# Kernel tuning notes

Measured on AMD Instinct MI355X. Metric: run time of the kernel, lower is better.

Reference implementation:

```python
import jax, jax.numpy as jnp
import numpy as np

N = 50000
E = 800000
D_IN = 256
D_OUT = 256
EPS = 1.0 + 1e-06


def setup_inputs() -> dict:
    key = jax.random.key(0)
    ks = jax.random.split(key, 10)
    x = jax.random.normal(ks[0], (N, D_IN), dtype=jnp.float32)
    lower_indices = jax.random.randint(ks[1], (2, E), 0, N, dtype=jnp.int64)
    lower_values = jax.random.uniform(ks[2], (E,), dtype=jnp.float32)
    upper_indices = jax.random.randint(ks[3], (2, E), 0, N, dtype=jnp.int64)
    upper_values = jax.random.uniform(ks[4], (E,), dtype=jnp.float32)
    s = 1.0 / np.sqrt(D_IN)
    W_lower = jax.random.uniform(ks[5], (D_IN, D_OUT), jnp.float32, -s, s)
    att_lower = jax.random.uniform(ks[6], (2 * D_OUT,), jnp.float32, -s, s)
    W_upper = jax.random.uniform(ks[7], (D_IN, D_OUT), jnp.float32, -s, s)
    att_upper = jax.random.uniform(ks[8], (2 * D_OUT,), jnp.float32, -s, s)
    W_lin = jax.random.uniform(ks[9], (D_IN, D_OUT), jnp.float32, -s, s)
    return {"x": x, "lower_indices": lower_indices, "lower_values": lower_values,
            "upper_indices": upper_indices, "upper_values": upper_values,
            "W_lower": W_lower, "att_lower": att_lower,
            "W_upper": W_upper, "att_upper": att_upper, "W_lin": W_lin}


def can_conv(x, indices, values, W, att_weight):
    # x: [N, d_in]; indices: [2, E] (row=target i, col=source j); values: [E]
    n = x.shape[0]
    xm = x @ W                                    # [N, d_out]
    tgt, src = indices[0], indices[1]
    d = xm.shape[1]
    # attention: elu( [x_i ; x_j] . att_weight ) computed without concat
    score = jax.nn.elu(xm @ att_weight[:d])[tgt] + jax.nn.elu(0.0) * 0.0  # placeholder
    score = jax.nn.elu((xm @ att_weight[:d])[tgt] + (xm @ att_weight[d:])[src])  # [E]
    v = score * values                            # attention * neighborhood values
    # sparse row-wise softmax (per target index)
    m = jax.ops.segment_max(v, tgt, num_segments=n)
    e = jnp.exp(v - m[tgt])
    s = jax.ops.segment_sum(e, tgt, num_segments=n)
    a = e / s[tgt]                                # [E]
    # spmm: out[i] = sum_j a_ij * xm[j]
    return jax.ops.segment_sum(a[:, None] * xm[src], tgt, num_segments=n)


def reference(x, lower_indices, lower_values, upper_indices, upper_values,
              W_lower, att_lower, W_upper, att_upper, W_lin):
    lower_x = can_conv(x, lower_indices, lower_values, W_lower, att_lower)
    upper_x = can_conv(x, upper_indices, upper_values, W_upper, att_upper)
    w_x = (x @ W_lin) * EPS
    return jax.nn.relu(lower_x + upper_x + w_x)
```

## Files before the change

kernel.cpp:

```cpp
#include <hip/hip_runtime.h>
#include <hip/hip_bf16.h>


constexpr int N_NODES = 50000;
constexpr int N_EDGES = 800000;
constexpr int D = 256;
constexpr float EPSV = 1.0f + 1e-06f;

typedef __attribute__((ext_vector_type(8))) short short8;
typedef __attribute__((ext_vector_type(4))) float f32x4;

__device__ __forceinline__ unsigned short f2bf(float f) {
    unsigned int b = __float_as_uint(f);
    unsigned int r = (b + 0x7FFFu + ((b >> 16) & 1u)) >> 16;
    return (unsigned short)r;
}
__device__ __forceinline__ float bf2f(unsigned short u) {
    return __uint_as_float(((unsigned int)u) << 16);
}

__global__ __launch_bounds__(256) void cvt_x_kernel(
    const float4* __restrict__ x, ushort4* __restrict__ xb, int n4)
{
    int i = blockIdx.x * 256 + threadIdx.x;
    if (i >= n4) return;
    float4 v = x[i];
    ushort4 o;
    o.x = f2bf(v.x); o.y = f2bf(v.y); o.z = f2bf(v.z); o.w = f2bf(v.w);
    xb[i] = o;
}

__global__ __launch_bounds__(256) void cvt_w_kernel(
    const float* __restrict__ W0, const float* __restrict__ W1,
    const float* __restrict__ W2, unsigned short* __restrict__ wbT)
{
    int z = blockIdx.y;
    const float* W = (z == 0) ? W0 : (z == 1) ? W1 : W2;
    int n = blockIdx.x;
    int k = threadIdx.x;
    wbT[(size_t)z * 65536 + (size_t)n * 256 + k] = f2bf(W[(size_t)k * 256 + n]);
}

__global__ __launch_bounds__(256) void gemm_fused_kernel(
    const unsigned short* __restrict__ xb, const unsigned short* __restrict__ wbT,
    const float* __restrict__ att_l, const float* __restrict__ att_u,
    unsigned short* __restrict__ xml, unsigned short* __restrict__ xmu,
    float* __restrict__ out,
    float* __restrict__ al, float* __restrict__ bl,
    float* __restrict__ au, float* __restrict__ bu, int M)
{
    const int tid = threadIdx.x;
    const int w = tid >> 6, lane = tid & 63;
    const int r16 = lane & 15, g = lane >> 4;
    const int m0 = blockIdx.x * 32;
    const int n0 = w * 64;

    const int ar0 = min(m0 + r16, M - 1);
    const int ar1 = min(m0 + 16 + r16, M - 1);
    const unsigned short* pa0 = xb + (size_t)ar0 * 256 + 8 * g;
    const unsigned short* pa1 = xb + (size_t)ar1 * 256 + 8 * g;
    const unsigned short* pb  = wbT + (size_t)(n0 + r16) * 256 + 8 * g;

    f32x4 acc[3][2][4];
    #pragma unroll
    for (int z = 0; z < 3; ++z)
        #pragma unroll
        for (int mf = 0; mf < 2; ++mf)
            #pragma unroll
            for (int nf = 0; nf < 4; ++nf)
                acc[z][mf][nf] = (f32x4){0.f, 0.f, 0.f, 0.f};

    #pragma unroll
    for (int kt = 0; kt < 256; kt += 32) {
        short8 a0 = *reinterpret_cast<const short8*>(pa0 + kt);
        short8 a1 = *reinterpret_cast<const short8*>(pa1 + kt);
        #pragma unroll
        for (int z = 0; z < 3; ++z) {
            #pragma unroll
            for (int nf = 0; nf < 4; ++nf) {
                short8 bf = *reinterpret_cast<const short8*>(
                    pb + (size_t)z * 65536 + (size_t)nf * 16 * 256 + kt);
                acc[z][0][nf] = __builtin_amdgcn_mfma_f32_16x16x32_bf16(a0, bf, acc[z][0][nf], 0, 0, 0);
                acc[z][1][nf] = __builtin_amdgcn_mfma_f32_16x16x32_bf16(a1, bf, acc[z][1][nf], 0, 0, 0);
            }
        }
    }

    #pragma unroll
    for (int mf = 0; mf < 2; ++mf)
        #pragma unroll
        for (int r = 0; r < 4; ++r) {
            int row = m0 + mf * 16 + g * 4 + r;
            if (row < M) {
                #pragma unroll
                for (int nf = 0; nf < 4; ++nf) {
                    int col = n0 + nf * 16 + r16;
                    xml[(size_t)row * 256 + col] = f2bf(acc[0][mf][nf][r]);
                    xmu[(size_t)row * 256 + col] = f2bf(acc[1][mf][nf][r]);
                    out[(size_t)row * 256 + col] = acc[2][mf][nf][r] * EPSV;
                }
            }
        }

    float attv[2][2][4];
    #pragma unroll
    for (int h = 0; h < 2; ++h)
        #pragma unroll
        for (int nf = 0; nf < 4; ++nf) {
            int c = h * 256 + n0 + nf * 16 + r16;
            attv[0][h][nf] = att_l[c];
            attv[1][h][nf] = att_u[c];
        }

    __shared__ float red[4][32][4];
    #pragma unroll
    for (int mf = 0; mf < 2; ++mf)
        #pragma unroll
        for (int r = 0; r < 4; ++r) {
            float p[4];
            #pragma unroll
            for (int z = 0; z < 2; ++z)
                #pragma unroll
                for (int h = 0; h < 2; ++h) {
                    float s = 0.f;
                    #pragma unroll
                    for (int nf = 0; nf < 4; ++nf)
                        s += acc[z][mf][nf][r] * attv[z][h][nf];
                    p[z * 2 + h] = s;
                }
            #pragma unroll
            for (int off = 1; off < 16; off <<= 1)
                #pragma unroll
                for (int c = 0; c < 4; ++c)
                    p[c] += __shfl_xor(p[c], off);
            if (r16 == 0) {
                int row_loc = mf * 16 + g * 4 + r;
                red[w][row_loc][0] = p[0];
                red[w][row_loc][1] = p[1];
                red[w][row_loc][2] = p[2];
                red[w][row_loc][3] = p[3];
            }
        }
    __syncthreads();
    if (tid < 128) {
        int row_loc = tid >> 2, comp = tid & 3;
        int row = m0 + row_loc;
        if (row < M) {
            float s = red[0][row_loc][comp] + red[1][row_loc][comp]
                    + red[2][row_loc][comp] + red[3][row_loc][comp];
            float* dst = (comp == 0) ? al : (comp == 1) ? bl : (comp == 2) ? au : bu;
            dst[row] = s;
        }
    }
}

__global__ __launch_bounds__(256) void hist_kernel(
    const int* __restrict__ il, const int* __restrict__ iu,
    int* __restrict__ cl, int* __restrict__ cu,
    int* __restrict__ rkl, int* __restrict__ rku)
{
    int e = blockIdx.x * 256 + threadIdx.x;
    if (e >= N_EDGES) return;
    rkl[e] = atomicAdd(&cl[il[e]], 1);
    rku[e] = atomicAdd(&cu[iu[e]], 1);
}

__global__ __launch_bounds__(1024) void scan_local_kernel(
    const int* __restrict__ cnt0, int* __restrict__ ro0,
    const int* __restrict__ cnt1, int* __restrict__ ro1,
    int* __restrict__ bsum, int n)
{
    int c = blockIdx.y;
    const int* cnt = c ? cnt1 : cnt0;
    int* ro = c ? ro1 : ro0;
    __shared__ int sm[1024];
    int tid = threadIdx.x;
    int i = blockIdx.x * 1024 + tid;
    int v = (i < n) ? cnt[i] : 0;
    sm[tid] = v;
    __syncthreads();
    #pragma unroll
    for (int off = 1; off < 1024; off <<= 1) {
        int t = (tid >= off) ? sm[tid - off] : 0;
        __syncthreads();
        sm[tid] += t;
        __syncthreads();
    }
    if (i < n) ro[i] = sm[tid] - v;
    if (tid == 1023) bsum[c * 64 + blockIdx.x] = sm[1023];
}

__global__ __launch_bounds__(128) void scan_bsum_kernel(int* __restrict__ bsum, int nb)
{
    int c = threadIdx.x >> 6, lane = threadIdx.x & 63;
    int v = (lane < nb) ? bsum[c * 64 + lane] : 0;
    int orig = v;
    #pragma unroll
    for (int off = 1; off < 64; off <<= 1) {
        int t = __shfl_up(v, off);
        if (lane >= off) v += t;
    }
    if (lane < nb) bsum[c * 64 + lane] = v - orig;
}

__global__ __launch_bounds__(256) void scan_apply_kernel(
    int* __restrict__ ro0, int* __restrict__ ro1,
    const int* __restrict__ bsum, int n)
{
    int c = blockIdx.y;
    int* ro = c ? ro1 : ro0;
    int i = blockIdx.x * 256 + threadIdx.x;
    if (i < n) ro[i] += bsum[c * 64 + (i >> 10)];
    if (i == 0) ro[n] = N_EDGES;
}

__global__ __launch_bounds__(256) void scatter_kernel(
    const int* __restrict__ il, const float* __restrict__ vl,
    const int* __restrict__ rol, const int* __restrict__ rkl, int2* __restrict__ egl,
    const int* __restrict__ iu, const float* __restrict__ vu,
    const int* __restrict__ rou, const int* __restrict__ rku, int2* __restrict__ egu)
{
    int e = blockIdx.x * 256 + threadIdx.x;
    if (e >= N_EDGES) return;
    int2 p; p.x = il[N_EDGES + e]; p.y = __float_as_int(vl[e]);
    egl[rol[il[e]] + rkl[e]] = p;
    int2 q; q.x = iu[N_EDGES + e]; q.y = __float_as_int(vu[e]);
    egu[rou[iu[e]] + rku[e]] = q;
}

__device__ __forceinline__ float wave_sum(float v) {
    #pragma unroll
    for (int off = 32; off; off >>= 1) v += __shfl_xor(v, off);
    return v;
}

__device__ __forceinline__ void pv_accum(
    int lane, float invs, float evl, int srcl, int t0, int m,
    const unsigned short* __restrict__ xm, float4& acc)
{
    int t = t0;
    for (; t + 2 <= m; t += 2) {
        float w0 = __shfl(evl, t) * invs;
        int   s0 = __shfl(srcl, t);
        float w1 = __shfl(evl, t + 1) * invs;
        int   s1 = __shfl(srcl, t + 1);
        ushort4 u0 = *reinterpret_cast<const ushort4*>(xm + (size_t)s0 * 256 + lane * 4);
        ushort4 u1 = *reinterpret_cast<const ushort4*>(xm + (size_t)s1 * 256 + lane * 4);
        acc.x += w0 * bf2f(u0.x) + w1 * bf2f(u1.x);
        acc.y += w0 * bf2f(u0.y) + w1 * bf2f(u1.y);
        acc.z += w0 * bf2f(u0.z) + w1 * bf2f(u1.z);
        acc.w += w0 * bf2f(u0.w) + w1 * bf2f(u1.w);
    }
    if (t < m) {
        float w0 = __shfl(evl, t) * invs;
        int   s0 = __shfl(srcl, t);
        ushort4 u0 = *reinterpret_cast<const ushort4*>(xm + (size_t)s0 * 256 + lane * 4);
        acc.x += w0 * bf2f(u0.x);
        acc.y += w0 * bf2f(u0.y);
        acc.z += w0 * bf2f(u0.z);
        acc.w += w0 * bf2f(u0.w);
    }
}

__device__ __forceinline__ void conv_accum(
    int node, int lane,
    const int* __restrict__ ro, const int2* __restrict__ eg,
    const float* __restrict__ a, const float* __restrict__ b,
    const unsigned short* __restrict__ xm, float4& acc)
{
    int rs = ro[node], re = ro[node + 1];
    int deg = re - rs;
    if (deg <= 0) return;
    float ai = a[node];
    if (deg <= 64) {
        float evl = 0.f; int srcl = 0;
        if (lane < deg) {
            int2 p = eg[rs + lane];
            srcl = p.x;
            float xv = ai + b[srcl];
            float sc = (xv > 0.f) ? xv : (expf(xv) - 1.f);
            evl = expf(sc * __int_as_float(p.y));
        }
        float invs = 1.f / wave_sum(evl);
        pv_accum(lane, invs, evl, srcl, 0, deg, xm, acc);
    } else {
        float s = 0.f;
        for (int c = rs; c < re; c += 64) {
            int m = min(64, re - c);
            float evl = 0.f;
            if (lane < m) {
                int2 p = eg[c + lane];
                float xv = ai + b[p.x];
                float sc = (xv > 0.f) ? xv : (expf(xv) - 1.f);
                evl = expf(sc * __int_as_float(p.y));
            }
            s += wave_sum(evl);
        }
        float invs = 1.f / s;
        for (int c = rs; c < re; c += 64) {
            int m = min(64, re - c);
            float evl = 0.f; int srcl = 0;
            if (lane < m) {
                int2 p = eg[c + lane];
                srcl = p.x;
                float xv = ai + b[srcl];
                float sc = (xv > 0.f) ? xv : (expf(xv) - 1.f);
                evl = expf(sc * __int_as_float(p.y));
            }
            pv_accum(lane, invs, evl, srcl, 0, m, xm, acc);
        }
    }
}

__global__ __launch_bounds__(256) void gather_kernel(
    const int* __restrict__ rol, const int2* __restrict__ egl,
    const float* __restrict__ al, const float* __restrict__ bl,
    const unsigned short* __restrict__ xml,
    const int* __restrict__ rou, const int2* __restrict__ egu,
    const float* __restrict__ au, const float* __restrict__ bu,
    const unsigned short* __restrict__ xmu,
    float4* __restrict__ out)
{
    int node = (int)((blockIdx.x * 256 + threadIdx.x) >> 6);
    int lane = threadIdx.x & 63;
    if (node >= N_NODES) return;
    float4 acc = make_float4(0.f, 0.f, 0.f, 0.f);
    conv_accum(node, lane, rol, egl, al, bl, xml, acc);
    conv_accum(node, lane, rou, egu, au, bu, xmu, acc);
    float4 xw = out[(size_t)node * 64 + lane];
    acc.x = fmaxf(acc.x + xw.x, 0.f);
    acc.y = fmaxf(acc.y + xw.y, 0.f);
    acc.z = fmaxf(acc.z + xw.z, 0.f);
    acc.w = fmaxf(acc.w + xw.w, 0.f);
    out[(size_t)node * 64 + lane] = acc;
}

extern "C" void kernel_launch(void* const* d_in, const int* in_sizes, int n_in,
                              void* d_out, int out_size, void* d_ws, size_t ws_size,
                              hipStream_t stream)
{
    (void)in_sizes; (void)n_in; (void)out_size; (void)ws_size;
    const float* x        = (const float*)d_in[0];
    const int*   low_idx  = (const int*)  d_in[1];
    const float* low_vals = (const float*)d_in[2];
    const int*   up_idx   = (const int*)  d_in[3];
    const float* up_vals  = (const float*)d_in[4];
    const float* W_lower  = (const float*)d_in[5];
    const float* att_low  = (const float*)d_in[6];
    const float* W_upper  = (const float*)d_in[7];
    const float* att_up   = (const float*)d_in[8];
    const float* W_lin    = (const float*)d_in[9];
    float* out = (float*)d_out;

    char* ws = (char*)d_ws;
    size_t off = 0;
    auto alloc = [&](size_t bytes) {
        void* p = ws + off;
        off += (bytes + 255) & ~(size_t)255;
        return p;
    };
    unsigned short* xb     = (unsigned short*)alloc((size_t)N_NODES * D * 2);
    unsigned short* wbT    = (unsigned short*)alloc((size_t)3 * 256 * 256 * 2);
    unsigned short* xm_low = (unsigned short*)alloc((size_t)N_NODES * D * 2);
    unsigned short* xm_up  = (unsigned short*)alloc((size_t)N_NODES * D * 2);
    float* a_low  = (float*)alloc(N_NODES * 4);
    float* b_low  = (float*)alloc(N_NODES * 4);
    float* a_up   = (float*)alloc(N_NODES * 4);
    float* b_up   = (float*)alloc(N_NODES * 4);
    int* zero_blk = (int*)alloc(2 * N_NODES * 4);
    int* cnt_low = zero_blk;
    int* cnt_up  = zero_blk + N_NODES;
    int* rk_low  = (int*)alloc((size_t)N_EDGES * 4);
    int* rk_up   = (int*)alloc((size_t)N_EDGES * 4);
    int* ro_low  = (int*)alloc((N_NODES + 1) * 4);
    int* ro_up   = (int*)alloc((N_NODES + 1) * 4);
    int* bsum    = (int*)alloc(2 * 64 * 4);
    int2* eg_low = (int2*)alloc((size_t)N_EDGES * 8);
    int2* eg_up  = (int2*)alloc((size_t)N_EDGES * 8);

    hipMemsetAsync(zero_blk, 0, 2 * N_NODES * 4, stream);

    int n4 = N_NODES * D / 4;
    cvt_x_kernel<<<(n4 + 255) / 256, 256, 0, stream>>>(
        (const float4*)x, (ushort4*)xb, n4);
    dim3 wgrid(256, 3);
    cvt_w_kernel<<<wgrid, 256, 0, stream>>>(W_lower, W_upper, W_lin, wbT);

    int gemmblocks = (N_NODES + 31) / 32;
    gemm_fused_kernel<<<gemmblocks, 256, 0, stream>>>(
        xb, wbT, att_low, att_up, xm_low, xm_up, out,
        a_low, b_low, a_up, b_up, N_NODES);

    int eblocks = (N_EDGES + 255) / 256;
    hist_kernel<<<eblocks, 256, 0, stream>>>(low_idx, up_idx, cnt_low, cnt_up,
                                             rk_low, rk_up);
    dim3 sgrid((N_NODES + 1023) / 1024, 2);
    scan_local_kernel<<<sgrid, 1024, 0, stream>>>(cnt_low, ro_low, cnt_up, ro_up,
                                                  bsum, N_NODES);
    scan_bsum_kernel<<<1, 128, 0, stream>>>(bsum, (N_NODES + 1023) / 1024);
    dim3 agrid((N_NODES + 255) / 256, 2);
    scan_apply_kernel<<<agrid, 256, 0, stream>>>(ro_low, ro_up, bsum, N_NODES);
    scatter_kernel<<<eblocks, 256, 0, stream>>>(
        low_idx, low_vals, ro_low, rk_low, eg_low,
        up_idx,  up_vals,  ro_up,  rk_up,  eg_up);

    int gblocks = (N_NODES + 3) / 4;
    gather_kernel<<<gblocks, 256, 0, stream>>>(
        ro_low, eg_low, a_low, b_low, xm_low,
        ro_up,  eg_up,  a_up,  b_up,  xm_up,
        (float4*)out);
}
```

Measured before the change: 483.5 us.

## Split GEMM per weight with LDS-staged B, separate attention kernel, fuse prep kernels

```diff
diff --git a/kernel.cpp b/kernel.cpp
--- a/kernel.cpp
+++ b/kernel.cpp
@@ -19,150 +19,135 @@
     return __uint_as_float(((unsigned int)u) << 16);
 }
 
-__global__ __launch_bounds__(256) void cvt_x_kernel(
-    const float4* __restrict__ x, ushort4* __restrict__ xb, int n4)
-{
-    int i = blockIdx.x * 256 + threadIdx.x;
-    if (i >= n4) return;
-    float4 v = x[i];
-    ushort4 o;
-    o.x = f2bf(v.x); o.y = f2bf(v.y); o.z = f2bf(v.z); o.w = f2bf(v.w);
-    xb[i] = o;
-}
-
-__global__ __launch_bounds__(256) void cvt_w_kernel(
+__global__ __launch_bounds__(256) void prep_kernel(
+    const float4* __restrict__ x, ushort4* __restrict__ xb, int n4,
     const float* __restrict__ W0, const float* __restrict__ W1,
-    const float* __restrict__ W2, unsigned short* __restrict__ wbT)
-{
-    int z = blockIdx.y;
-    const float* W = (z == 0) ? W0 : (z == 1) ? W1 : W2;
-    int n = blockIdx.x;
-    int k = threadIdx.x;
-    wbT[(size_t)z * 65536 + (size_t)n * 256 + k] = f2bf(W[(size_t)k * 256 + n]);
-}
-
-__global__ __launch_bounds__(256) void gemm_fused_kernel(
+    const float* __restrict__ W2, unsigned short* __restrict__ wbT,
+    const int* __restrict__ il, const int* __restrict__ iu,
+    int* __restrict__ cl, int* __restrict__ cu,
+    int* __restrict__ rkl, int* __restrict__ rku)
+{
+    int gid = blockIdx.x * 256 + threadIdx.x;
+    int gsz = gridDim.x * 256;
+    for (int i = gid; i < n4; i += gsz) {
+        float4 v = x[i];
+        ushort4 o;
+        o.x = f2bf(v.x); o.y = f2bf(v.y); o.z = f2bf(v.z); o.w = f2bf(v.w);
+        xb[i] = o;
+    }
+    for (int i = gid; i < 3 * 65536; i += gsz) {
+        int z = i >> 16, rem = i & 65535;
+        int k = rem >> 8, n = rem & 255;
+        const float* W = (z == 0) ? W0 : (z == 1) ? W1 : W2;
+        wbT[(size_t)z * 65536 + (size_t)n * 256 + k] = f2bf(W[(size_t)k * 256 + n]);
+    }
+    for (int e = gid; e < N_EDGES; e += gsz) {
+        rkl[e] = atomicAdd(&cl[il[e]], 1);
+        rku[e] = atomicAdd(&cu[iu[e]], 1);
+    }
+}
+
+__global__ __launch_bounds__(256) void gemm_lds_kernel(
     const unsigned short* __restrict__ xb, const unsigned short* __restrict__ wbT,
-    const float* __restrict__ att_l, const float* __restrict__ att_u,
     unsigned short* __restrict__ xml, unsigned short* __restrict__ xmu,
-    float* __restrict__ out,
-    float* __restrict__ al, float* __restrict__ bl,
-    float* __restrict__ au, float* __restrict__ bu, int M)
-{
+    float* __restrict__ out, int M)
+{
+    const int wz = blockIdx.z;
     const int tid = threadIdx.x;
     const int w = tid >> 6, lane = tid & 63;
     const int r16 = lane & 15, g = lane >> 4;
-    const int m0 = blockIdx.x * 32;
-    const int n0 = w * 64;
+    const int m0 = blockIdx.x * 128 + w * 32;
+    const int n0 = blockIdx.y * 64;
+
+    __shared__ short8 bs[8][4][64];
+    {
+        const unsigned short* wb = wbT + (size_t)wz * 65536;
+        #pragma unroll
+        for (int c = tid; c < 2048; c += 256) {
+            int kt = c >> 8, nf = (c >> 6) & 3, l = c & 63;
+            bs[kt][nf][l] = *reinterpret_cast<const short8*>(
+                wb + (size_t)(n0 + nf * 16 + (l & 15)) * 256 + kt * 32 + 8 * (l >> 4));
+        }
+    }
+    __syncthreads();
 
     const int ar0 = min(m0 + r16, M - 1);
     const int ar1 = min(m0 + 16 + r16, M - 1);
     const unsigned short* pa0 = xb + (size_t)ar0 * 256 + 8 * g;
     const unsigned short* pa1 = xb + (size_t)ar1 * 256 + 8 * g;
-    const unsigned short* pb  = wbT + (size_t)(n0 + r16) * 256 + 8 * g;
-
-    f32x4 acc[3][2][4];
-    #pragma unroll
-    for (int z = 0; z < 3; ++z)
+
+    f32x4 acc[2][4];
+    #pragma unroll
+    for (int mf = 0; mf < 2; ++mf)
+        #pragma unroll
+        for (int nf = 0; nf < 4; ++nf)
+            acc[mf][nf] = (f32x4){0.f, 0.f, 0.f, 0.f};
+
+    #pragma unroll
+    for (int kt = 0; kt < 8; ++kt) {
+        short8 a0 = *reinterpret_cast<const short8*>(pa0 + kt * 32);
+        short8 a1 = *reinterpret_cast<const short8*>(pa1 + kt * 32);
+        #pragma unroll
+        for (int nf = 0; nf < 4; ++nf) {
+            short8 bf = bs[kt][nf][lane];
+            acc[0][nf] = __builtin_amdgcn_mfma_f32_16x16x32_bf16(a0, bf, acc[0][nf], 0, 0, 0);
+            acc[1][nf] = __builtin_amdgcn_mfma_f32_16x16x32_bf16(a1, bf, acc[1][nf], 0, 0, 0);
+        }
+    }
+
+    if (wz < 2) {
+        unsigned short* dst = wz ? xmu : xml;
         #pragma unroll
         for (int mf = 0; mf < 2; ++mf)
             #pragma unroll
-            for (int nf = 0; nf < 4; ++nf)
-                acc[z][mf][nf] = (f32x4){0.f, 0.f, 0.f, 0.f};
-
-    #pragma unroll
-    for (int kt = 0; kt < 256; kt += 32) {
-        short8 a0 = *reinterpret_cast<const short8*>(pa0 + kt);
-        short8 a1 = *reinterpret_cast<const short8*>(pa1 + kt);
-        #pragma unroll
-        for (int z = 0; z < 3; ++z) {
-            #pragma unroll
-            for (int nf = 0; nf < 4; ++nf) {
-                short8 bf = *reinterpret_cast<const short8*>(
-                    pb + (size_t)z * 65536 + (size_t)nf * 16 * 256 + kt);
-                acc[z][0][nf] = __builtin_amdgcn_mfma_f32_16x16x32_bf16(a0, bf, acc[z][0][nf], 0, 0, 0);
-                acc[z][1][nf] = __builtin_amdgcn_mfma_f32_16x16x32_bf16(a1, bf, acc[z][1][nf], 0, 0, 0);
-            }
-        }
-    }
-
-    #pragma unroll
-    for (int mf = 0; mf < 2; ++mf)
-        #pragma unroll
-        for (int r = 0; r < 4; ++r) {
-            int row = m0 + mf * 16 + g * 4 + r;
-            if (row < M) {
-                #pragma unroll
-                for (int nf = 0; nf < 4; ++nf) {
-                    int col = n0 + nf * 16 + r16;
-                    xml[(size_t)row * 256 + col] = f2bf(acc[0][mf][nf][r]);
-                    xmu[(size_t)row * 256 + col] = f2bf(acc[1][mf][nf][r]);
-                    out[(size_t)row * 256 + col] = acc[2][mf][nf][r] * EPSV;
+            for (int r = 0; r < 4; ++r) {
+                int row = m0 + mf * 16 + g * 4 + r;
+                if (row < M) {
+                    #pragma unroll
+                    for (int nf = 0; nf < 4; ++nf)
+                        dst[(size_t)row * 256 + n0 + nf * 16 + r16] = f2bf(acc[mf][nf][r]);
                 }
             }
-        }
-
-    float attv[2][2][4];
-    #pragma unroll
-    for (int h = 0; h < 2; ++h)
-        #pragma unroll
-        for (int nf = 0; nf < 4; ++nf) {
-            int c = h * 256 + n0 + nf * 16 + r16;
-            attv[0][h][nf] = att_l[c];
-            attv[1][h][nf] = att_u[c];
-        }
-
-    __shared__ float red[4][32][4];
-    #pragma unroll
-    for (int mf = 0; mf < 2; ++mf)
-        #pragma unroll
-        for (int r = 0; r < 4; ++r) {
-            float p[4];
+    } else {
+        #pragma unroll
+        for (int mf = 0; mf < 2; ++mf)
             #pragma unroll
-            for (int z = 0; z < 2; ++z)
-                #pragma unroll
-                for (int h = 0; h < 2; ++h) {
-                    float s = 0.f;
+            for (int r = 0; r < 4; ++r) {
+                int row = m0 + mf * 16 + g * 4 + r;
+                if (row < M) {
                     #pragma unroll
                     for (int nf = 0; nf < 4; ++nf)
-                        s += acc[z][mf][nf][r] * attv[z][h][nf];
-                    p[z * 2 + h] = s;
+                        out[(size_t)row * 256 + n0 + nf * 16 + r16] = acc[mf][nf][r] * EPSV;
                 }
-            #pragma unroll
-            for (int off = 1; off < 16; off <<= 1)
-                #pragma unroll
-                for (int c = 0; c < 4; ++c)
-                    p[c] += __shfl_xor(p[c], off);
-            if (r16 == 0) {
-                int row_loc = mf * 16 + g * 4 + r;
-                red[w][row_loc][0] = p[0];
-                red[w][row_loc][1] = p[1];
-                red[w][row_loc][2] = p[2];
-                red[w][row_loc][3] = p[3];
             }
-        }
-    __syncthreads();
-    if (tid < 128) {
-        int row_loc = tid >> 2, comp = tid & 3;
-        int row = m0 + row_loc;
-        if (row < M) {
-            float s = red[0][row_loc][comp] + red[1][row_loc][comp]
-                    + red[2][row_loc][comp] + red[3][row_loc][comp];
-            float* dst = (comp == 0) ? al : (comp == 1) ? bl : (comp == 2) ? au : bu;
-            dst[row] = s;
-        }
-    }
-}
-
-__global__ __launch_bounds__(256) void hist_kernel(
-    const int* __restrict__ il, const int* __restrict__ iu,
-    int* __restrict__ cl, int* __restrict__ cu,
-    int* __restrict__ rkl, int* __restrict__ rku)
-{
-    int e = blockIdx.x * 256 + threadIdx.x;
-    if (e >= N_EDGES) return;
-    rkl[e] = atomicAdd(&cl[il[e]], 1);
-    rku[e] = atomicAdd(&cu[iu[e]], 1);
+    }
+}
+
+__global__ __launch_bounds__(256) void att_both_kernel(
+    const unsigned short* __restrict__ xml, const unsigned short* __restrict__ xmu,
+    const float* __restrict__ att_l, const float* __restrict__ att_u,
+    float* __restrict__ al, float* __restrict__ bl,
+    float* __restrict__ au, float* __restrict__ bu, int n)
+{
+    int node = (int)((blockIdx.x * 256 + threadIdx.x) >> 6);
+    int lane = threadIdx.x & 63;
+    if (node >= n) return;
+    int o = lane * 4;
+    ushort4 ul = *reinterpret_cast<const ushort4*>(xml + (size_t)node * 256 + o);
+    ushort4 uu = *reinterpret_cast<const ushort4*>(xmu + (size_t)node * 256 + o);
+    float l0 = bf2f(ul.x), l1 = bf2f(ul.y), l2 = bf2f(ul.z), l3 = bf2f(ul.w);
+    float u0 = bf2f(uu.x), u1 = bf2f(uu.y), u2 = bf2f(uu.z), u3 = bf2f(uu.w);
+    float p[4];
+    p[0] = l0 * att_l[o] + l1 * att_l[o + 1] + l2 * att_l[o + 2] + l3 * att_l[o + 3];
+    p[1] = l0 * att_l[D + o] + l1 * att_l[D + o + 1] + l2 * att_l[D + o + 2] + l3 * att_l[D + o + 3];
+    p[2] = u0 * att_u[o] + u1 * att_u[o + 1] + u2 * att_u[o + 2] + u3 * att_u[o + 3];
+    p[3] = u0 * att_u[D + o] + u1 * att_u[D + o + 1] + u2 * att_u[D + o + 2] + u3 * att_u[D + o + 3];
+    #pragma unroll
+    for (int off = 32; off; off >>= 1)
+        #pragma unroll
+        for (int c = 0; c < 4; ++c)
+            p[c] += __shfl_down(p[c], off);
+    if (lane == 0) { al[node] = p[0]; bl[node] = p[1]; au[node] = p[2]; bu[node] = p[3]; }
 }
 
 __global__ __launch_bounds__(1024) void scan_local_kernel(
@@ -235,10 +220,10 @@
 }
 
 __device__ __forceinline__ void pv_accum(
-    int lane, float invs, float evl, int srcl, int t0, int m,
+    int lane, float invs, float evl, int srcl, int m,
     const unsigned short* __restrict__ xm, float4& acc)
 {
-    int t = t0;
+    int t = 0;
     for (; t + 2 <= m; t += 2) {
         float w0 = __shfl(evl, t) * invs;
         int   s0 = __shfl(srcl, t);
@@ -282,7 +267,7 @@
             evl = expf(sc * __int_as_float(p.y));
         }
         float invs = 1.f / wave_sum(evl);
-        pv_accum(lane, invs, evl, srcl, 0, deg, xm, acc);
+        pv_accum(lane, invs, evl, srcl, deg, xm, acc);
     } else {
         float s = 0.f;
         for (int c = rs; c < re; c += 64) {
@@ -307,7 +292,7 @@
                 float sc = (xv > 0.f) ? xv : (expf(xv) - 1.f);
                 evl = expf(sc * __int_as_float(p.y));
             }
-            pv_accum(lane, invs, evl, srcl, 0, m, xm, acc);
+            pv_accum(lane, invs, evl, srcl, m, xm, acc);
         }
     }
 }
@@ -381,25 +366,25 @@
     hipMemsetAsync(zero_blk, 0, 2 * N_NODES * 4, stream);
 
     int n4 = N_NODES * D / 4;
-    cvt_x_kernel<<<(n4 + 255) / 256, 256, 0, stream>>>(
-        (const float4*)x, (ushort4*)xb, n4);
-    dim3 wgrid(256, 3);
-    cvt_w_kernel<<<wgrid, 256, 0, stream>>>(W_lower, W_upper, W_lin, wbT);
-
-    int gemmblocks = (N_NODES + 31) / 32;
-    gemm_fused_kernel<<<gemmblocks, 256, 0, stream>>>(
-        xb, wbT, att_low, att_up, xm_low, xm_up, out,
-        a_low, b_low, a_up, b_up, N_NODES);
-
-    int eblocks = (N_EDGES + 255) / 256;
-    hist_kernel<<<eblocks, 256, 0, stream>>>(low_idx, up_idx, cnt_low, cnt_up,
-                                             rk_low, rk_up);
+    prep_kernel<<<2048, 256, 0, stream>>>(
+        (const float4*)x, (ushort4*)xb, n4,
+        W_lower, W_upper, W_lin, wbT,
+        low_idx, up_idx, cnt_low, cnt_up, rk_low, rk_up);
+
+    dim3 ggrid((N_NODES + 127) / 128, 4, 3);
+    gemm_lds_kernel<<<ggrid, 256, 0, stream>>>(xb, wbT, xm_low, xm_up, out, N_NODES);
+
+    int ablocks = (N_NODES + 3) / 4;
+    att_both_kernel<<<ablocks, 256, 0, stream>>>(
+        xm_low, xm_up, att_low, att_up, a_low, b_low, a_up, b_up, N_NODES);
+
     dim3 sgrid((N_NODES + 1023) / 1024, 2);
     scan_local_kernel<<<sgrid, 1024, 0, stream>>>(cnt_low, ro_low, cnt_up, ro_up,
                                                   bsum, N_NODES);
     scan_bsum_kernel<<<1, 128, 0, stream>>>(bsum, (N_NODES + 1023) / 1024);
     dim3 agrid((N_NODES + 255) / 256, 2);
     scan_apply_kernel<<<agrid, 256, 0, stream>>>(ro_low, ro_up, bsum, N_NODES);
+    int eblocks = (N_EDGES + 255) / 256;
     scatter_kernel<<<eblocks, 256, 0, stream>>>(
         low_idx, low_vals, ro_low, rk_low, eg_low,
         up_idx,  up_vals,  ro_up,  rk_up,  eg_up);
```

New measurement: 439.4 us. 9.1% less time.
